# Performance work log

Hardware: AMD Instinct MI355X
Metric: run time of the kernel (lower is better)

## Reference

```python
import jax, jax.numpy as jnp
import numpy as np

NUM_EMBEDDINGS = 1024
EMBEDDING_DIM = 256
COMMITMENT_COST = 0.25


def setup_inputs() -> dict:
    key = jax.random.key(0)
    k_z, k_e = jax.random.split(key)
    z = jax.random.normal(k_z, (8, EMBEDDING_DIM, 16, 16, 16), dtype=jnp.float32)
    # nn.Embedding weight initialized uniform(-1/K, 1/K)
    codebook = jax.random.uniform(
        k_e, (NUM_EMBEDDINGS, EMBEDDING_DIM), dtype=jnp.float32,
        minval=-1.0 / NUM_EMBEDDINGS, maxval=1.0 / NUM_EMBEDDINGS)
    return {"z": z, "codebook": codebook}


def reference(z, codebook):
    B, D, H, W, L = z.shape
    # (B, D, H, W, L) -> (B, H, W, L, D) -> (N, D)
    z_perm = jnp.transpose(z, (0, 2, 3, 4, 1))          # (B,H,W,L,D)
    z_flat = z_perm.reshape(-1, D)                       # (N,D)
    # squared-distance via expansion: ||z||^2 + ||e||^2 - 2 z.e^T
    distances = ((z_flat ** 2).sum(axis=1, keepdims=True)
                 + (codebook ** 2).sum(axis=1)
                 - 2.0 * z_flat @ codebook.T)            # (N,K)
    indices = jnp.argmin(distances, axis=1)              # (N,)
    quantized = codebook[indices].reshape(B, H, W, L, D)
    idx_out = indices.reshape(B, H, W, L)
    # losses (stop_gradient mirrors .detach())
    e_latent_loss = jnp.mean((jax.lax.stop_gradient(quantized) - z_perm) ** 2)
    q_latent_loss = jnp.mean((quantized - jax.lax.stop_gradient(z_perm)) ** 2)
    vq_loss = q_latent_loss + COMMITMENT_COST * e_latent_loss
    # straight-through estimator
    quant_st = z_perm + jax.lax.stop_gradient(quantized - z_perm)
    quant_out = jnp.transpose(quant_st, (0, 4, 1, 2, 3))  # (B,D,H,W,L)
    return quant_out, idx_out, vq_loss
```

## Files before the change

### kernel.cpp

```cpp
#include <hip/hip_runtime.h>


#define K_CODES 1024
#define DIM 256
#define N_TOK 32768
#define SPATIAL 4096
#define TOK_BLK 32
#define NBLK (N_TOK / TOK_BLK)
#define CAP 28
#define MARGIN 1e-3f

typedef __attribute__((ext_vector_type(8))) short short8;
typedef __attribute__((ext_vector_type(4))) float float4v;

#define WS_LOSS 0
#define WS_CNT 8
#define WS_E2 16
#define WS_EB 2048

#define O_IDX (8 * DIM * SPATIAL)
#define O_LOSS (O_IDX + N_TOK)

__device__ __forceinline__ short f2bf(float v) {
  unsigned u = __float_as_uint(v);
  u = (u + 0x7fffu + ((u >> 16) & 1u)) >> 16;
  return (short)u;
}

__global__ __launch_bounds__(256) void prep_kernel(const float* __restrict__ e,
                                                   float* __restrict__ ws) {
  __shared__ float sq[DIM];
  __shared__ __align__(16) short sbf[DIM];
  __shared__ float chv[16];
  int k = blockIdx.x, d = threadIdx.x;
  float v = e[k * DIM + d];
  sbf[d] = f2bf(v);
  sq[d] = __fmul_rn(v, v);
  __syncthreads();
  if (d < 32) {
    int f = d >> 2, q = d & 3;
    int stage = k >> 6, ct = (k >> 4) & 3, nn = k & 15;
    short8 chunk = *(const short8*)(sbf + f * 32 + q * 8);
    int off8 = ((stage * 4 + ct) * 8 + f) * 64 + q * 16 + nn;
    ((short8*)(ws + WS_EB))[off8] = chunk;
  }
  if (d < 16) {
    int blkb = d >> 3, j = d & 7;
    const float* x = sq + blkb * 128;
    float c = x[j];
#pragma unroll
    for (int i = 1; i < 16; i++) c = __fadd_rn(c, x[i * 8 + j]);
    chv[d] = c;
  }
  __syncthreads();
  if (d == 0) {
    float a0 = __fadd_rn(__fadd_rn(chv[0], chv[1]), __fadd_rn(chv[2], chv[3]));
    float a1 = __fadd_rn(__fadd_rn(chv[4], chv[5]), __fadd_rn(chv[6], chv[7]));
    float resA = __fadd_rn(a0, a1);
    float b0 = __fadd_rn(__fadd_rn(chv[8], chv[9]), __fadd_rn(chv[10], chv[11]));
    float b1 = __fadd_rn(__fadd_rn(chv[12], chv[13]), __fadd_rn(chv[14], chv[15]));
    float resB = __fadd_rn(b0, b1);
    ws[WS_E2 + k] = __fadd_rn(resA, resB);
    if (k == 0) {
      ws[WS_LOSS] = 0.f;
      ((unsigned*)ws)[WS_CNT] = 0u;
    }
  }
}

__global__ __launch_bounds__(256, 4) void main_kernel(const float* __restrict__ z,
                                                      const float* __restrict__ e,
                                                      float* __restrict__ ws,
                                                      float* __restrict__ out) {
  __shared__ unsigned short cand[TOK_BLK][CAP];
  __shared__ float cands[TOK_BLK][CAP];
  __shared__ float aminv[2][TOK_BLK];
  __shared__ int cnt[TOK_BLK];
  __shared__ float Szs[TOK_BLK];
  __shared__ int mini_sh[TOK_BLK];
  __shared__ float red[4];

  int tid = threadIdx.x, w = tid >> 6, lane = tid & 63;
  int quad = lane >> 4, nn = lane & 15;
  int g = w & 1, kh = w >> 1;
  int n0 = blockIdx.x * TOK_BLK;
  int b = n0 >> 12, s0 = n0 & 4095;
  const float* zb = z + (size_t)b * DIM * SPATIAL + s0;
  const float* Se = ws + WS_E2;
  const short8* eBf = (const short8*)(ws + WS_EB);
  if (tid < TOK_BLK) cnt[tid] = 0;
  __syncthreads();

  {
    int tt = tid >> 3, m = tid & 7;
    int blkb = m >> 2, j0 = (2 * m) & 7;
    const float* zp = zb + tt;
    float v0 = zp[(size_t)(blkb * 128 + j0) * SPATIAL];
    float v1 = zp[(size_t)(blkb * 128 + j0 + 1) * SPATIAL];
    float r0 = __fmul_rn(v0, v0), r1 = __fmul_rn(v1, v1);
    for (int i = 1; i < 16; i++) {
      v0 = zp[(size_t)(blkb * 128 + i * 8 + j0) * SPATIAL];
      v1 = zp[(size_t)(blkb * 128 + i * 8 + j0 + 1) * SPATIAL];
      r0 = __fadd_rn(r0, __fmul_rn(v0, v0));
      r1 = __fadd_rn(r1, __fmul_rn(v1, v1));
    }
    float p = __fadd_rn(r0, r1);
    float q1 = __fadd_rn(p, __shfl_xor(p, 1, 8));
    float q2 = __fadd_rn(q1, __shfl_xor(q1, 2, 8));
    float tot = __fadd_rn(q2, __shfl_xor(q2, 4, 8));
    if (m == 0) Szs[tt] = tot;
  }

  int tokA = g * 16 + nn;
  short8 A[8];
#pragma unroll
  for (int f = 0; f < 8; f++) {
    short8 a;
#pragma unroll
    for (int j = 0; j < 8; j++) {
      int d = f * 32 + quad * 8 + j;
      a[j] = f2bf(zb[(size_t)d * SPATIAL + tokA]);
    }
    A[f] = a;
  }

  float thr[4] = {3.4e38f, 3.4e38f, 3.4e38f, 3.4e38f};
  for (int s8 = 0; s8 < 8; s8++) {
    int stage = kh * 8 + s8;
    for (int ct = 0; ct < 4; ct++) {
      int kbase = stage * 64 + ct * 16;
      float4v C = {0.f, 0.f, 0.f, 0.f};
      const short8* Bp = eBf + (size_t)((stage * 4 + ct) * 8) * 64;
#pragma unroll
      for (int f = 0; f < 8; f++) {
        short8 Bf = Bp[f * 64 + lane];
        C = __builtin_amdgcn_mfma_f32_16x16x32_bf16(A[f], Bf, C, 0, 0, 0);
      }
      float SeK = Se[kbase + nn];
      float sv[4];
      bool pr[4];
#pragma unroll
      for (int r = 0; r < 4; r++) {
        float s = fmaf(-2.f, C[r], SeK);
        float m = s;
        m = fminf(m, __shfl_xor(m, 1, 16));
        m = fminf(m, __shfl_xor(m, 2, 16));
        m = fminf(m, __shfl_xor(m, 4, 16));
        m = fminf(m, __shfl_xor(m, 8, 16));
        thr[r] = fminf(thr[r], m);
        sv[r] = s;
        pr[r] = s < thr[r] + MARGIN;
      }
      if (__ballot(pr[0] | pr[1] | pr[2] | pr[3])) {
#pragma unroll
        for (int r = 0; r < 4; r++) {
          unsigned long long bl = __ballot(pr[r]);
          unsigned grp = (unsigned)((bl >> (quad * 16)) & 0xffffULL);
          if (grp) {
            int tb = g * 16 + quad * 4 + r;
            int base = 0;
            if (nn == 0) base = atomicAdd(&cnt[tb], __popc(grp));
            base = __shfl(base, quad * 16);
            if (pr[r]) {
              int pos = base + __popc(grp & ((1u << nn) - 1u));
              if (pos < CAP) {
                cand[tb][pos] = (unsigned short)(kbase + nn);
                cands[tb][pos] = sv[r];
              }
            }
          }
        }
      }
    }
  }
#pragma unroll
  for (int r = 0; r < 4; r++)
    if (nn == 0) aminv[kh][g * 16 + quad * 4 + r] = thr[r];
  __syncthreads();

  int tl = lane >> 3, oct = lane & 7;
  int tb = w * 8 + tl;
  int cc = cnt[tb];
  int cl = cc < CAP ? cc : CAP;
  float bestD = 3.4e38f;
  int bestk = 0x7fffffff;
  {
    const float* zp = zb + tb;
    float amin = fminf(aminv[0][tb], aminv[1][tb]);
    float Szn = Szs[tb];
    for (int c = oct; c < cl; c += 8) {
      if (cands[tb][c] >= amin + MARGIN) continue;
      int k = cand[tb][c];
      const float* er = e + (size_t)k * DIM;
      float acc = 0.f;
#pragma unroll 4
      for (int dd = 0; dd < DIM; dd += 4) {
        float4 e4 = *(const float4*)(er + dd);
        acc = fmaf(zp[(size_t)(dd + 0) * SPATIAL], e4.x, acc);
        acc = fmaf(zp[(size_t)(dd + 1) * SPATIAL], e4.y, acc);
        acc = fmaf(zp[(size_t)(dd + 2) * SPATIAL], e4.z, acc);
        acc = fmaf(zp[(size_t)(dd + 3) * SPATIAL], e4.w, acc);
      }
      float D = __fsub_rn(__fadd_rn(Szn, Se[k]), __fmul_rn(2.f, acc));
      if (D < bestD || (D == bestD && k < bestk)) { bestD = D; bestk = k; }
    }
  }
#pragma unroll
  for (int off = 4; off >= 1; off >>= 1) {
    float oD = __shfl_down(bestD, off, 8);
    int ok = __shfl_down(bestk, off, 8);
    if (oD < bestD || (oD == bestD && ok < bestk)) { bestD = oD; bestk = ok; }
  }
  if (oct == 0 && cc <= CAP) {
    mini_sh[tb] = bestk;
    out[O_IDX + n0 + tb] = (float)bestk;
  }
  for (int t = 0; t < 8; t++) {
    int tb2 = w * 8 + t;
    if (cnt[tb2] > CAP) {
      const float* zq = zb + tb2;
      float Szn = Szs[tb2];
      float bD = 3.4e38f;
      int bk = 0x7fffffff;
      for (int k = lane; k < K_CODES; k += 64) {
        const float* er = e + (size_t)k * DIM;
        float acc = 0.f;
#pragma unroll 4
        for (int dd = 0; dd < DIM; dd += 4) {
          float4 e4 = *(const float4*)(er + dd);
          acc = fmaf(zq[(size_t)(dd + 0) * SPATIAL], e4.x, acc);
          acc = fmaf(zq[(size_t)(dd + 1) * SPATIAL], e4.y, acc);
          acc = fmaf(zq[(size_t)(dd + 2) * SPATIAL], e4.z, acc);
          acc = fmaf(zq[(size_t)(dd + 3) * SPATIAL], e4.w, acc);
        }
        float D = __fsub_rn(__fadd_rn(Szn, Se[k]), __fmul_rn(2.f, acc));
        if (D < bD || (D == bD && k < bk)) { bD = D; bk = k; }
      }
#pragma unroll
      for (int m = 1; m < 64; m <<= 1) {
        float oD = __shfl_xor(bD, m);
        int ok = __shfl_xor(bk, m);
        if (oD < bD || (oD == bD && ok < bk)) { bD = oD; bk = ok; }
      }
      if (lane == 0) {
        mini_sh[tb2] = bk;
        out[O_IDX + n0 + tb2] = (float)bk;
      }
    }
  }
  __syncthreads();

  int h = lane >> 5, t = lane & 31;
  int mten = mini_sh[t];
  const float* erow = e + (size_t)mten * DIM;
  float* op = out + (size_t)b * DIM * SPATIAL + s0;
  float sumsq = 0.f;
#pragma unroll 2
  for (int i4 = 0; i4 < 32; i4 += 4) {
    int d0 = w * 64 + h * 32 + i4;
    float4 v4 = *(const float4*)(erow + d0);
#pragma unroll
    for (int m = 0; m < 4; m++) {
      float v = (m == 0) ? v4.x : (m == 1) ? v4.y : (m == 2) ? v4.z : v4.w;
      float zv = zb[(size_t)(d0 + m) * SPATIAL + t];
      float df = __fsub_rn(v, zv);
      sumsq = fmaf(df, df, sumsq);
      op[(size_t)(d0 + m) * SPATIAL + t] = v;
    }
  }
#pragma unroll
  for (int o = 32; o > 0; o >>= 1) sumsq += __shfl_down(sumsq, o, 64);
  if (lane == 0) red[w] = sumsq;
  __syncthreads();
  if (tid == 0) {
    atomicAdd(ws + WS_LOSS, red[0] + red[1] + red[2] + red[3]);
    __threadfence();
    unsigned tcnt = atomicAdd((unsigned*)ws + WS_CNT, 1u);
    if (tcnt == NBLK - 1) {
      float total = atomicAdd(ws + WS_LOSS, 0.f);
      out[O_LOSS] = 1.25f * total / 8388608.f;
    }
  }
}

extern "C" void kernel_launch(void* const* d_in, const int* in_sizes, int n_in,
                              void* d_out, int out_size, void* d_ws, size_t ws_size,
                              hipStream_t stream) {
  const float* z = (const float*)d_in[0];
  const float* e = (const float*)d_in[1];
  float* ws = (float*)d_ws;
  float* out = (float*)d_out;

  prep_kernel<<<K_CODES, 256, 0, stream>>>(e, ws);
  main_kernel<<<NBLK, 256, 0, stream>>>(z, e, ws, out);
}
```

Baseline: 218.5 us.

## Double token tile per block and stage bf16 codebook through LDS

Each block now handles 64 tokens with 512 threads. The bf16 codebook is staged stage by stage into a 32KB shared buffer, so every B fragment loaded from global memory is reused by four token groups instead of being fetched per wave. The token norm is split into partial sums across the two code-halves, and the epilogue is remapped to 64 tokens per wave. This adds two barriers per stage and raises shared memory use, which may reduce occupancy.

```diff
diff --git a/kernel.cpp b/kernel.cpp
--- a/kernel.cpp
+++ b/kernel.cpp
@@ -5,7 +5,7 @@
 #define DIM 256
 #define N_TOK 32768
 #define SPATIAL 4096
-#define TOK_BLK 32
+#define TOK_BLK 64
 #define NBLK (N_TOK / TOK_BLK)
 #define CAP 28
 #define MARGIN 1e-3f
@@ -68,47 +68,49 @@
   }
 }
 
-__global__ __launch_bounds__(256, 4) void main_kernel(const float* __restrict__ z,
+__global__ __launch_bounds__(512, 4) void main_kernel(const float* __restrict__ z,
                                                       const float* __restrict__ e,
                                                       float* __restrict__ ws,
                                                       float* __restrict__ out) {
+  __shared__ __align__(16) short Bst[64 * 256];
   __shared__ unsigned short cand[TOK_BLK][CAP];
   __shared__ float cands[TOK_BLK][CAP];
   __shared__ float aminv[2][TOK_BLK];
   __shared__ int cnt[TOK_BLK];
-  __shared__ float Szs[TOK_BLK];
+  __shared__ float Szp[2][TOK_BLK];
   __shared__ int mini_sh[TOK_BLK];
-  __shared__ float red[4];
+  __shared__ float red[8];
 
   int tid = threadIdx.x, w = tid >> 6, lane = tid & 63;
   int quad = lane >> 4, nn = lane & 15;
-  int g = w & 1, kh = w >> 1;
+  int g = w & 3, kh = w >> 2;
   int n0 = blockIdx.x * TOK_BLK;
   int b = n0 >> 12, s0 = n0 & 4095;
   const float* zb = z + (size_t)b * DIM * SPATIAL + s0;
   const float* Se = ws + WS_E2;
-  const short8* eBf = (const short8*)(ws + WS_EB);
+  const uint4* eBg = (const uint4*)(ws + WS_EB);
   if (tid < TOK_BLK) cnt[tid] = 0;
-  __syncthreads();
 
   {
-    int tt = tid >> 3, m = tid & 7;
-    int blkb = m >> 2, j0 = (2 * m) & 7;
-    const float* zp = zb + tt;
-    float v0 = zp[(size_t)(blkb * 128 + j0) * SPATIAL];
-    float v1 = zp[(size_t)(blkb * 128 + j0 + 1) * SPATIAL];
-    float r0 = __fmul_rn(v0, v0), r1 = __fmul_rn(v1, v1);
-    for (int i = 1; i < 16; i++) {
-      v0 = zp[(size_t)(blkb * 128 + i * 8 + j0) * SPATIAL];
-      v1 = zp[(size_t)(blkb * 128 + i * 8 + j0 + 1) * SPATIAL];
-      r0 = __fadd_rn(r0, __fmul_rn(v0, v0));
-      r1 = __fadd_rn(r1, __fmul_rn(v1, v1));
+    const float* zp = zb + g * 16 + nn;
+    float r0, r1;
+    {
+      int j0 = quad * 2;
+      float v0 = zp[(size_t)(kh * 128 + j0) * SPATIAL];
+      float v1 = zp[(size_t)(kh * 128 + j0 + 1) * SPATIAL];
+      r0 = __fmul_rn(v0, v0);
+      r1 = __fmul_rn(v1, v1);
+      for (int i = 1; i < 16; i++) {
+        v0 = zp[(size_t)(kh * 128 + i * 8 + j0) * SPATIAL];
+        v1 = zp[(size_t)(kh * 128 + i * 8 + j0 + 1) * SPATIAL];
+        r0 = __fadd_rn(r0, __fmul_rn(v0, v0));
+        r1 = __fadd_rn(r1, __fmul_rn(v1, v1));
+      }
     }
     float p = __fadd_rn(r0, r1);
-    float q1 = __fadd_rn(p, __shfl_xor(p, 1, 8));
-    float q2 = __fadd_rn(q1, __shfl_xor(q1, 2, 8));
-    float tot = __fadd_rn(q2, __shfl_xor(q2, 4, 8));
-    if (m == 0) Szs[tt] = tot;
+    float s1 = __fadd_rn(p, __shfl_xor(p, 16));
+    float s2 = __fadd_rn(s1, __shfl_xor(s1, 32));
+    if (quad == 0) Szp[kh][g * 16 + nn] = s2;
   }
 
   int tokA = g * 16 + nn;
@@ -125,12 +127,18 @@
   }
 
   float thr[4] = {3.4e38f, 3.4e38f, 3.4e38f, 3.4e38f};
-  for (int s8 = 0; s8 < 8; s8++) {
-    int stage = kh * 8 + s8;
-    for (int ct = 0; ct < 4; ct++) {
+  for (int stage = 0; stage < 16; stage++) {
+    __syncthreads();
+#pragma unroll
+    for (int i = 0; i < 4; i++)
+      ((uint4*)Bst)[i * 512 + tid] = eBg[(size_t)stage * 2048 + i * 512 + tid];
+    __syncthreads();
+
+    for (int ctl = 0; ctl < 2; ctl++) {
+      int ct = kh * 2 + ctl;
       int kbase = stage * 64 + ct * 16;
       float4v C = {0.f, 0.f, 0.f, 0.f};
-      const short8* Bp = eBf + (size_t)((stage * 4 + ct) * 8) * 64;
+      const short8* Bp = (const short8*)Bst + ct * 8 * 64;
 #pragma unroll
       for (int f = 0; f < 8; f++) {
         short8 Bf = Bp[f * 64 + lane];
@@ -184,10 +192,10 @@
   int cl = cc < CAP ? cc : CAP;
   float bestD = 3.4e38f;
   int bestk = 0x7fffffff;
+  float SznT = __fadd_rn(Szp[0][tb], Szp[1][tb]);
   {
     const float* zp = zb + tb;
     float amin = fminf(aminv[0][tb], aminv[1][tb]);
-    float Szn = Szs[tb];
     for (int c = oct; c < cl; c += 8) {
       if (cands[tb][c] >= amin + MARGIN) continue;
       int k = cand[tb][c];
@@ -201,7 +209,7 @@
         acc = fmaf(zp[(size_t)(dd + 2) * SPATIAL], e4.z, acc);
         acc = fmaf(zp[(size_t)(dd + 3) * SPATIAL], e4.w, acc);
       }
-      float D = __fsub_rn(__fadd_rn(Szn, Se[k]), __fmul_rn(2.f, acc));
+      float D = __fsub_rn(__fadd_rn(SznT, Se[k]), __fmul_rn(2.f, acc));
       if (D < bestD || (D == bestD && k < bestk)) { bestD = D; bestk = k; }
     }
   }
@@ -219,7 +227,7 @@
     int tb2 = w * 8 + t;
     if (cnt[tb2] > CAP) {
       const float* zq = zb + tb2;
-      float Szn = Szs[tb2];
+      float Szn = __fadd_rn(Szp[0][tb2], Szp[1][tb2]);
       float bD = 3.4e38f;
       int bk = 0x7fffffff;
       for (int k = lane; k < K_CODES; k += 64) {
@@ -250,22 +258,21 @@
   }
   __syncthreads();
 
-  int h = lane >> 5, t = lane & 31;
-  int mten = mini_sh[t];
+  int mten = mini_sh[lane];
   const float* erow = e + (size_t)mten * DIM;
   float* op = out + (size_t)b * DIM * SPATIAL + s0;
   float sumsq = 0.f;
 #pragma unroll 2
   for (int i4 = 0; i4 < 32; i4 += 4) {
-    int d0 = w * 64 + h * 32 + i4;
-    float4 v4 = *(const float4*)(erow + d0);
+    int d = w * 32 + i4;
+    float4 v4 = *(const float4*)(erow + d);
 #pragma unroll
     for (int m = 0; m < 4; m++) {
       float v = (m == 0) ? v4.x : (m == 1) ? v4.y : (m == 2) ? v4.z : v4.w;
-      float zv = zb[(size_t)(d0 + m) * SPATIAL + t];
+      float zv = zb[(size_t)(d + m) * SPATIAL + lane];
       float df = __fsub_rn(v, zv);
       sumsq = fmaf(df, df, sumsq);
-      op[(size_t)(d0 + m) * SPATIAL + t] = v;
+      op[(size_t)(d + m) * SPATIAL + lane] = v;
     }
   }
 #pragma unroll
@@ -273,10 +280,12 @@
   if (lane == 0) red[w] = sumsq;
   __syncthreads();
   if (tid == 0) {
-    atomicAdd(ws + WS_LOSS, red[0] + red[1] + red[2] + red[3]);
+    float rs = ((red[0] + red[1]) + (red[2] + red[3])) +
+               ((red[4] + red[5]) + (red[6] + red[7]));
+    atomicAdd(ws + WS_LOSS, rs);
     __threadfence();
-    unsigned tcnt = atomicAdd((unsigned*)ws + WS_CNT, 1u);
-    if (tcnt == NBLK - 1) {
+    unsigned t = atomicAdd((unsigned*)ws + WS_CNT, 1u);
+    if (t == NBLK - 1) {
       float total = atomicAdd(ws + WS_LOSS, 0.f);
       out[O_LOSS] = 1.25f * total / 8388608.f;
     }
@@ -292,5 +301,5 @@
   float* out = (float*)d_out;
 
   prep_kernel<<<K_CODES, 256, 0, stream>>>(e, ws);
-  main_kernel<<<NBLK, 256, 0, stream>>>(z, e, ws, out);
+  main_kernel<<<NBLK, 512, 0, stream>>>(z, e, ws, out);
 }
```

After: 203.4 us. -6.9%, faster.
